# Kernel optimization log

Hardware: AMD Instinct MI355X
Metric: run time of the kernel (lower is better)

## Reference

```python
import jax, jax.numpy as jnp
import numpy as np

N, D, H, C = 100000, 128, 8, 16  # nodes, units=H*C, heads, per-head channels
E = 400000                        # edges per edge set (2 edge sets)
LN_EPS = 1e-3                     # keras LayerNormalization default epsilon


def setup_inputs() -> dict:
    key = jax.random.key(0)
    ks = jax.random.split(key, 16)
    def dense(k, i, o):
        return jax.random.normal(k, (i, o), jnp.float32) / np.float32(np.sqrt(i))
    return dict(
        x=jax.random.normal(ks[0], (N, D), jnp.float32),
        src0=jax.random.randint(ks[1], (E,), 0, N),
        dst0=jax.random.randint(ks[2], (E,), 0, N),
        src1=jax.random.randint(ks[3], (E,), 0, N),
        dst1=jax.random.randint(ks[4], (E,), 0, N),
        Wk=dense(ks[5], D, D), bk=jnp.zeros((D,), jnp.float32),
        Wm=dense(ks[6], D, D), bm=jnp.zeros((D,), jnp.float32),
        Wq=dense(ks[7], D, D), bq=jnp.zeros((D,), jnp.float32),
        Wa=dense(ks[8], D, D), ba=jnp.zeros((D,), jnp.float32),
        Watt0=jax.random.normal(ks[9], (H, C, C), jnp.float32) / np.float32(np.sqrt(C)),
        Wmsg0=jax.random.normal(ks[10], (H, C, C), jnp.float32) / np.float32(np.sqrt(C)),
        Watt1=jax.random.normal(ks[11], (H, C, C), jnp.float32) / np.float32(np.sqrt(C)),
        Wmsg1=jax.random.normal(ks[12], (H, C, C), jnp.float32) / np.float32(np.sqrt(C)),
        prior0=jnp.ones((H,), jnp.float32),
        prior1=jnp.ones((H,), jnp.float32),
        skip=jnp.ones((), jnp.float32),
        gamma=jnp.ones((D,), jnp.float32),
        beta=jnp.zeros((D,), jnp.float32),
    )


def reference(x, src0, dst0, src1, dst1, Wk, bk, Wm, bm, Wq, bq, Wa, ba,
              Watt0, Wmsg0, Watt1, Wmsg1, prior0, prior1, skip, gamma, beta):
    # Node-level projections, split per head: [N, H, C]
    k = (x @ Wk + bk).reshape(N, H, C)
    m = (x @ Wm + bm).reshape(N, H, C)
    q = (x @ Wq + bq).reshape(N, H, C)
    scale = 1.0 / jnp.sqrt(jnp.float32(C))

    def edge_terms(src, dst, Watt, Wmsg, prior):
        # per-edge-type relation projections of gathered sender keys/messages
        ke = jnp.einsum('ehk,hkl->ehl', k[src], Watt)          # [E, H, C]
        score = jnp.einsum('ehl,ehl->eh', ke, q[dst]) * prior * scale  # [E, H]
        msg = jnp.einsum('ehk,hkl->ehl', m[src], Wmsg)          # [E, H, C]
        return score, msg

    s0, m0 = edge_terms(src0, dst0, Watt0, Wmsg0, prior0)
    s1, m1 = edge_terms(src1, dst1, Watt1, Wmsg1, prior1)

    # Joint segment softmax over all incoming edges (both edge sets) per receiver
    scores = jnp.concatenate([s0, s1], axis=0)   # [2E, H]
    msgs = jnp.concatenate([m0, m1], axis=0)     # [2E, H, C]
    recv = jnp.concatenate([dst0, dst1], axis=0)

    smax = jax.ops.segment_max(scores, recv, num_segments=N)   # [N, H]
    ex = jnp.exp(scores - smax[recv])
    denom = jax.ops.segment_sum(ex, recv, num_segments=N)      # [N, H]
    d_e = denom[recv]
    attn = ex / jnp.where(d_e > 0, d_e, 1.0)                   # [2E, H]

    pooled = jax.ops.segment_sum(attn[:, :, None] * msgs, recv,
                                 num_segments=N).reshape(N, D)  # [N, D]

    # aggr(gelu(pooled)); weighted skip; layer norm
    h = jax.nn.gelu(pooled, approximate=False) @ Wa + ba
    alpha = jax.nn.sigmoid(skip)
    out = alpha * h + (1.0 - alpha) * x
    mu = jnp.mean(out, axis=-1, keepdims=True)
    var = jnp.var(out, axis=-1, keepdims=True)
    out = (out - mu) * jax.lax.rsqrt(var + LN_EPS) * gamma + beta
    return out
```

## Files before the change

### kernel.cpp

```cpp
#include <hip/hip_runtime.h>
#include <hip/hip_bf16.h>
#include <math.h>

#define N_NODES 100000
#define DIM 128
#define NH 8
#define NC 16
#define E_EDGES 400000
#define LN_EPS 1e-3f
#define SCAN_B 1024

typedef __attribute__((ext_vector_type(8))) short short8v;
typedef __attribute__((ext_vector_type(4))) float float4v;

__device__ __forceinline__ short bf16bits(float v) {
    __hip_bfloat16 b = __float2bfloat16(v);
    return *(short*)&b;
}

__global__ __launch_bounds__(128) void fuse_weights(
    const float* __restrict__ Wk, const float* __restrict__ bk,
    const float* __restrict__ Wm, const float* __restrict__ bm,
    const float* __restrict__ Wq, const float* __restrict__ bq,
    const float* __restrict__ Wa, const float* __restrict__ ba,
    const float* __restrict__ Watt0, const float* __restrict__ Wmsg0,
    const float* __restrict__ Watt1, const float* __restrict__ Wmsg1,
    const float* __restrict__ prior0, const float* __restrict__ prior1,
    __hip_bfloat16* __restrict__ Wt, float* __restrict__ bias)
{
    const int c = blockIdx.x;
    const int d = threadIdx.x;
    const int sec = c >> 7, j = c & 127, h = j >> 4, l = j & 15;
    float v, b;
    if (sec == 4)      { v = Wq[d * DIM + j]; b = bq[j]; }
    else if (sec == 5) { v = Wa[d * DIM + j]; b = ba[j]; }
    else {
        const float* W1 = (sec < 2) ? Wk : Wm;
        const float* bs = (sec < 2) ? bk : bm;
        const float* W2 = (sec == 0) ? Watt0 : (sec == 1) ? Watt1
                          : (sec == 2) ? Wmsg0 : Wmsg1;
        float scale = (sec == 0) ? prior0[h] * 0.25f
                    : (sec == 1) ? prior1[h] * 0.25f : 1.f;
        float s = 0.f, sb = 0.f;
        #pragma unroll
        for (int kk = 0; kk < NC; ++kk) {
            float w2 = W2[h * 256 + kk * 16 + l];
            s  = fmaf(W1[d * DIM + h * 16 + kk], w2, s);
            sb = fmaf(bs[h * 16 + kk], w2, sb);
        }
        v = s * scale; b = sb * scale;
    }
    Wt[(size_t)c * DIM + d] = __float2bfloat16(v);
    if (d == 0) bias[c] = b;
}

__global__ __launch_bounds__(256) void proj_mfma(
    const float* __restrict__ x,
    const __hip_bfloat16* __restrict__ Wt,
    const float* __restrict__ bias,
    __hip_bfloat16* __restrict__ kattC,
    __hip_bfloat16* __restrict__ mmsgC,
    __hip_bfloat16* __restrict__ qb)
{
    __shared__ short tile[32][DIM];
    const int wave = threadIdx.x >> 6, lane = threadIdx.x & 63;
    const int quad = lane >> 4, mcol = lane & 15;
    const int r0 = blockIdx.x * 32;

    short8v a0[4], a1[4];
    const float* xr0 = x + (size_t)(r0 + mcol) * DIM + quad * 8;
    const float* xr1 = xr0 + 16 * DIM;
    #pragma unroll
    for (int kb = 0; kb < 4; ++kb) {
        #pragma unroll
        for (int jj = 0; jj < 8; ++jj) {
            a0[kb][jj] = bf16bits(xr0[kb * 32 + jj]);
            a1[kb][jj] = bf16bits(xr1[kb * 32 + jj]);
        }
    }

    const int wrow = threadIdx.x >> 3;
    const int wcol = (threadIdx.x & 7) * 16;
    #pragma unroll
    for (int s = 0; s < 5; ++s) {
        #pragma unroll
        for (int tp = 0; tp < 2; ++tp) {
            const int ct = (wave + tp * 4) * 16;
            const int c0 = s * 128 + ct;
            const short* wp = (const short*)Wt + (size_t)(c0 + mcol) * DIM + quad * 8;
            float4v acc0 = {0.f, 0.f, 0.f, 0.f};
            float4v acc1 = {0.f, 0.f, 0.f, 0.f};
            #pragma unroll
            for (int kb = 0; kb < 4; ++kb) {
                short8v bfr = *(const short8v*)(wp + kb * 32);
                acc0 = __builtin_amdgcn_mfma_f32_16x16x32_bf16(a0[kb], bfr, acc0, 0, 0, 0);
                acc1 = __builtin_amdgcn_mfma_f32_16x16x32_bf16(a1[kb], bfr, acc1, 0, 0, 0);
            }
            const float bcol = bias[c0 + mcol];
            const int cc = ct + mcol, rq = quad * 4;
            #pragma unroll
            for (int g = 0; g < 4; ++g) {
                tile[rq + g][cc]      = bf16bits(acc0[g] + bcol);
                tile[rq + 16 + g][cc] = bf16bits(acc1[g] + bcol);
            }
        }
        __syncthreads();
        __hip_bfloat16* dst =
            (s == 0) ? kattC + (size_t)r0 * DIM :
            (s == 1) ? kattC + ((size_t)N_NODES + r0) * DIM :
            (s == 2) ? mmsgC + (size_t)r0 * DIM :
            (s == 3) ? mmsgC + ((size_t)N_NODES + r0) * DIM :
                       qb    + (size_t)r0 * DIM;
        short* dp = (short*)dst + (size_t)wrow * DIM + wcol;
        *(short8v*)dp       = *(short8v*)&tile[wrow][wcol];
        *(short8v*)(dp + 8) = *(short8v*)&tile[wrow][wcol + 8];
        __syncthreads();
    }
}

__global__ __launch_bounds__(256) void hist_kernel(
    const int* __restrict__ dst0, const int* __restrict__ dst1,
    int* __restrict__ counts)
{
    int e = blockIdx.x * 256 + threadIdx.x;
    if (e < E_EDGES) atomicAdd(&counts[dst0[e]], 1);
    int e1 = e - E_EDGES;
    if (e1 >= 0 && e1 < E_EDGES) atomicAdd(&counts[dst1[e1]], 1);
}

__global__ __launch_bounds__(SCAN_B) void scanA_kernel(
    const int* __restrict__ counts, int* __restrict__ row_ptr,
    int* __restrict__ bsum)
{
    __shared__ int buf[2][SCAN_B];
    int i = blockIdx.x * SCAN_B + threadIdx.x;
    int v = (i < N_NODES) ? counts[i] : 0;
    int cur = 0;
    buf[0][threadIdx.x] = v;
    __syncthreads();
    #pragma unroll
    for (int off = 1; off < SCAN_B; off <<= 1) {
        int t = buf[cur][threadIdx.x];
        int add = (threadIdx.x >= off) ? buf[cur][threadIdx.x - off] : 0;
        buf[cur ^ 1][threadIdx.x] = t + add;
        cur ^= 1;
        __syncthreads();
    }
    int inc = buf[cur][threadIdx.x];
    if (i < N_NODES) row_ptr[i] = inc - v;
    if (threadIdx.x == SCAN_B - 1) bsum[blockIdx.x] = inc;
}

__global__ __launch_bounds__(128) void scanB_kernel(int* __restrict__ bsum, int nblocks)
{
    __shared__ int buf[2][128];
    int t = threadIdx.x;
    int v = (t < nblocks) ? bsum[t] : 0;
    buf[0][t] = v;
    __syncthreads();
    int cur = 0;
    #pragma unroll
    for (int off = 1; off < 128; off <<= 1) {
        int a = buf[cur][t];
        if (t >= off) a += buf[cur][t - off];
        buf[cur ^ 1][t] = a;
        cur ^= 1;
        __syncthreads();
    }
    if (t < nblocks) bsum[t] = buf[cur][t] - v;
}

__global__ __launch_bounds__(SCAN_B) void scanC_kernel(
    int* __restrict__ row_ptr, int* __restrict__ cursor,
    const int* __restrict__ bsum)
{
    int i = blockIdx.x * SCAN_B + threadIdx.x;
    if (i < N_NODES) {
        int r = row_ptr[i] + bsum[blockIdx.x];
        row_ptr[i] = r;
        cursor[i] = r;
    }
}

__global__ __launch_bounds__(256) void scatter_kernel(
    const int* __restrict__ src0, const int* __restrict__ dst0,
    const int* __restrict__ src1, const int* __restrict__ dst1,
    int* __restrict__ cursor, unsigned int* __restrict__ eidx)
{
    int e = blockIdx.x * 256 + threadIdx.x;
    if (e < E_EDGES) {
        int d = dst0[e];
        int pos = atomicAdd(&cursor[d], 1);
        eidx[pos] = (unsigned int)src0[e];
    }
    int e1 = e - E_EDGES;
    if (e1 >= 0 && e1 < E_EDGES) {
        int d = dst1[e1];
        int pos = atomicAdd(&cursor[d], 1);
        eidx[pos] = (unsigned int)(src1[e1] + N_NODES);
    }
}

__global__ __launch_bounds__(256) void agg_kernel(
    const __hip_bfloat162* __restrict__ katt,
    const __hip_bfloat162* __restrict__ mmsg,
    const __hip_bfloat162* __restrict__ qb2,
    const int* __restrict__ row_ptr, const int* __restrict__ counts,
    const unsigned int* __restrict__ eidx,
    __hip_bfloat162* __restrict__ pooled2)
{
    const int wave = threadIdx.x >> 6, lane = threadIdx.x & 63;
    const int n = blockIdx.x * 4 + wave;
    if (n >= N_NODES) return;
    const int start = row_ptr[n], cnt = counts[n];
    __hip_bfloat162 qv = qb2[(size_t)n * 64 + lane];
    const float qx = __bfloat162float(qv.x), qy = __bfloat162float(qv.y);

    float accx = 0.f, accy = 0.f, den = 0.f;
    int i = 0;
    for (; i + 2 <= cnt; i += 2) {
        unsigned int r0 = eidx[start + i];
        unsigned int r1 = eidx[start + i + 1];
        __hip_bfloat162 ka0 = katt[(size_t)r0 * 64 + lane];
        __hip_bfloat162 ka1 = katt[(size_t)r1 * 64 + lane];
        __hip_bfloat162 mg0 = mmsg[(size_t)r0 * 64 + lane];
        __hip_bfloat162 mg1 = mmsg[(size_t)r1 * 64 + lane];
        float p0 = fmaf(__bfloat162float(ka0.x), qx,
                        __bfloat162float(ka0.y) * qy);
        float p1 = fmaf(__bfloat162float(ka1.x), qx,
                        __bfloat162float(ka1.y) * qy);
        p0 += __shfl_xor(p0, 1, 64); p0 += __shfl_xor(p0, 2, 64); p0 += __shfl_xor(p0, 4, 64);
        p1 += __shfl_xor(p1, 1, 64); p1 += __shfl_xor(p1, 2, 64); p1 += __shfl_xor(p1, 4, 64);
        float e0 = __expf(p0), e1 = __expf(p1);
        accx = fmaf(e0, __bfloat162float(mg0.x), accx);
        accy = fmaf(e0, __bfloat162float(mg0.y), accy);
        accx = fmaf(e1, __bfloat162float(mg1.x), accx);
        accy = fmaf(e1, __bfloat162float(mg1.y), accy);
        den += e0 + e1;
    }
    if (i < cnt) {
        unsigned int r0 = eidx[start + i];
        __hip_bfloat162 ka0 = katt[(size_t)r0 * 64 + lane];
        __hip_bfloat162 mg0 = mmsg[(size_t)r0 * 64 + lane];
        float p0 = fmaf(__bfloat162float(ka0.x), qx,
                        __bfloat162float(ka0.y) * qy);
        p0 += __shfl_xor(p0, 1, 64); p0 += __shfl_xor(p0, 2, 64); p0 += __shfl_xor(p0, 4, 64);
        float e0 = __expf(p0);
        accx = fmaf(e0, __bfloat162float(mg0.x), accx);
        accy = fmaf(e0, __bfloat162float(mg0.y), accy);
        den += e0;
    }

    float vx = 0.f, vy = 0.f;
    if (den > 0.f) { vx = accx / den; vy = accy / den; }
    vx = 0.5f * vx * (1.f + erff(vx * 0.70710678118654752f));
    vy = 0.5f * vy * (1.f + erff(vy * 0.70710678118654752f));
    __hip_bfloat162 o; o.x = __float2bfloat16(vx); o.y = __float2bfloat16(vy);
    pooled2[(size_t)n * 64 + lane] = o;
}

__global__ __launch_bounds__(256) void final_mfma(
    const __hip_bfloat16* __restrict__ pooled,
    const __hip_bfloat16* __restrict__ Wt,
    const float* __restrict__ bias,
    const float* __restrict__ x,
    const float* __restrict__ skip, const float* __restrict__ gamma,
    const float* __restrict__ beta, float* __restrict__ out)
{
    __shared__ float hs[32][DIM];
    const int wave = threadIdx.x >> 6, lane = threadIdx.x & 63;
    const int quad = lane >> 4, mcol = lane & 15;
    const int r0 = blockIdx.x * 32;

    short8v a0[4], a1[4];
    const short* pp0 = (const short*)pooled + (size_t)(r0 + mcol) * DIM + quad * 8;
    const short* pp1 = pp0 + 16 * DIM;
    #pragma unroll
    for (int kb = 0; kb < 4; ++kb) {
        a0[kb] = *(const short8v*)(pp0 + kb * 32);
        a1[kb] = *(const short8v*)(pp1 + kb * 32);
    }
    const float alpha = 1.f / (1.f + expf(-skip[0]));

    #pragma unroll
    for (int t = 0; t < 2; ++t) {
        const int c0 = wave * 32 + t * 16;
        const short* wp = (const short*)Wt + (size_t)(640 + c0 + mcol) * DIM + quad * 8;
        float4v acc0 = {0.f, 0.f, 0.f, 0.f};
        float4v acc1 = {0.f, 0.f, 0.f, 0.f};
        #pragma unroll
        for (int kb = 0; kb < 4; ++kb) {
            short8v bfr = *(const short8v*)(wp + kb * 32);
            acc0 = __builtin_amdgcn_mfma_f32_16x16x32_bf16(a0[kb], bfr, acc0, 0, 0, 0);
            acc1 = __builtin_amdgcn_mfma_f32_16x16x32_bf16(a1[kb], bfr, acc1, 0, 0, 0);
        }
        const float bcol = bias[640 + c0 + mcol];
        const int cc = c0 + mcol;
        const int rq = quad * 4;
        #pragma unroll
        for (int g = 0; g < 4; ++g) {
            int rA = rq + g, rB = rq + 16 + g;
            hs[rA][cc] = alpha * (acc0[g] + bcol)
                       + (1.f - alpha) * x[(size_t)(r0 + rA) * DIM + cc];
            hs[rB][cc] = alpha * (acc1[g] + bcol)
                       + (1.f - alpha) * x[(size_t)(r0 + rB) * DIM + cc];
        }
    }
    __syncthreads();

    float gam0 = gamma[lane], gam1 = gamma[lane + 64];
    float bet0 = beta[lane],  bet1 = beta[lane + 64];
    for (int r = wave; r < 32; r += 4) {
        int row = r0 + r;
        float v0 = hs[r][lane], v1 = hs[r][lane + 64];
        float s = v0 + v1, s2 = v0 * v0 + v1 * v1;
        #pragma unroll
        for (int off = 1; off < 64; off <<= 1) {
            s  += __shfl_xor(s,  off, 64);
            s2 += __shfl_xor(s2, off, 64);
        }
        float mu = s * (1.f / 128.f);
        float var = s2 * (1.f / 128.f) - mu * mu;
        float rstd = rsqrtf(var + LN_EPS);
        out[(size_t)row * DIM + lane]      = (v0 - mu) * rstd * gam0 + bet0;
        out[(size_t)row * DIM + lane + 64] = (v1 - mu) * rstd * gam1 + bet1;
    }
}

extern "C" void kernel_launch(void* const* d_in, const int* in_sizes, int n_in,
                              void* d_out, int out_size, void* d_ws, size_t ws_size,
                              hipStream_t stream) {
    const float* x     = (const float*)d_in[0];
    const int*   src0  = (const int*)d_in[1];
    const int*   dst0  = (const int*)d_in[2];
    const int*   src1  = (const int*)d_in[3];
    const int*   dst1  = (const int*)d_in[4];
    const float* Wk    = (const float*)d_in[5];
    const float* bk    = (const float*)d_in[6];
    const float* Wm    = (const float*)d_in[7];
    const float* bm    = (const float*)d_in[8];
    const float* Wq    = (const float*)d_in[9];
    const float* bq    = (const float*)d_in[10];
    const float* Wa    = (const float*)d_in[11];
    const float* ba    = (const float*)d_in[12];
    const float* Watt0 = (const float*)d_in[13];
    const float* Wmsg0 = (const float*)d_in[14];
    const float* Watt1 = (const float*)d_in[15];
    const float* Wmsg1 = (const float*)d_in[16];
    const float* prior0= (const float*)d_in[17];
    const float* prior1= (const float*)d_in[18];
    const float* skip  = (const float*)d_in[19];
    const float* gamma = (const float*)d_in[20];
    const float* beta  = (const float*)d_in[21];
    float* out = (float*)d_out;

    const size_t nd = (size_t)N_NODES * DIM;
    char* wsb = (char*)d_ws;
    __hip_bfloat16* Wt    = (__hip_bfloat16*)wsb;  wsb += (size_t)768 * DIM * 2;
    float* bias           = (float*)wsb;           wsb += 768 * 4;
    __hip_bfloat16* kattC = (__hip_bfloat16*)wsb;  wsb += 2 * nd * 2;
    __hip_bfloat16* mmsgC = (__hip_bfloat16*)wsb;  wsb += 2 * nd * 2;
    __hip_bfloat16* qb    = (__hip_bfloat16*)wsb;  wsb += nd * 2;
    __hip_bfloat16* pooled= (__hip_bfloat16*)wsb;  wsb += nd * 2;
    int* counts  = (int*)wsb;                      wsb += (size_t)N_NODES * 4;
    int* row_ptr = (int*)wsb;                      wsb += (size_t)N_NODES * 4;
    int* cursor  = (int*)wsb;                      wsb += (size_t)N_NODES * 4;
    int* bsum    = (int*)wsb;                      wsb += 128 * 4;
    unsigned int* eidx = (unsigned int*)wsb;

    hipMemsetAsync(counts, 0, (size_t)N_NODES * 4, stream);

    const int scan_blocks = (N_NODES + SCAN_B - 1) / SCAN_B;
    const int edge_blocks = (2 * E_EDGES + 255) / 256;

    hist_kernel<<<dim3(edge_blocks), dim3(256), 0, stream>>>(dst0, dst1, counts);
    scanA_kernel<<<dim3(scan_blocks), dim3(SCAN_B), 0, stream>>>(counts, row_ptr, bsum);
    scanB_kernel<<<dim3(1), dim3(128), 0, stream>>>(bsum, scan_blocks);
    scanC_kernel<<<dim3(scan_blocks), dim3(SCAN_B), 0, stream>>>(row_ptr, cursor, bsum);
    scatter_kernel<<<dim3(edge_blocks), dim3(256), 0, stream>>>(
        src0, dst0, src1, dst1, cursor, eidx);

    fuse_weights<<<dim3(768), dim3(128), 0, stream>>>(
        Wk, bk, Wm, bm, Wq, bq, Wa, ba,
        Watt0, Wmsg0, Watt1, Wmsg1, prior0, prior1, Wt, bias);
    proj_mfma<<<dim3(N_NODES / 32), dim3(256), 0, stream>>>(
        x, Wt, bias, kattC, mmsgC, qb);

    agg_kernel<<<dim3((N_NODES + 3) / 4), dim3(256), 0, stream>>>(
        (const __hip_bfloat162*)kattC, (const __hip_bfloat162*)mmsgC,
        (const __hip_bfloat162*)qb, row_ptr, counts, eidx,
        (__hip_bfloat162*)pooled);

    final_mfma<<<dim3(N_NODES / 32), dim3(256), 0, stream>>>(
        pooled, Wt, bias, x, skip, gamma, beta, out);
}
```

Before: 415.3 us.

## Drop scanC pass, use per-wave staging tiles, unroll aggregation loop by four

After: 420.2 us. No clear change (+1.2%).

```diff
diff --git a/kernel.cpp b/kernel.cpp
--- a/kernel.cpp
+++ b/kernel.cpp
@@ -62,31 +62,38 @@
     __hip_bfloat16* __restrict__ mmsgC,
     __hip_bfloat16* __restrict__ qb)
 {
-    __shared__ short tile[32][DIM];
+    __shared__ short tile[4][32][40];
     const int wave = threadIdx.x >> 6, lane = threadIdx.x & 63;
     const int quad = lane >> 4, mcol = lane & 15;
     const int r0 = blockIdx.x * 32;
 
     short8v a0[4], a1[4];
-    const float* xr0 = x + (size_t)(r0 + mcol) * DIM + quad * 8;
-    const float* xr1 = xr0 + 16 * DIM;
-    #pragma unroll
-    for (int kb = 0; kb < 4; ++kb) {
-        #pragma unroll
-        for (int jj = 0; jj < 8; ++jj) {
-            a0[kb][jj] = bf16bits(xr0[kb * 32 + jj]);
-            a1[kb][jj] = bf16bits(xr1[kb * 32 + jj]);
-        }
-    }
-
-    const int wrow = threadIdx.x >> 3;
-    const int wcol = (threadIdx.x & 7) * 16;
+    {
+        const float4* xp0 = (const float4*)(x + (size_t)(r0 + mcol) * DIM + quad * 8);
+        const float4* xp1 = (const float4*)(x + (size_t)(r0 + 16 + mcol) * DIM + quad * 8);
+        #pragma unroll
+        for (int kb = 0; kb < 4; ++kb) {
+            float4 u0 = xp0[kb * 8], v0 = xp0[kb * 8 + 1];
+            float4 u1 = xp1[kb * 8], v1 = xp1[kb * 8 + 1];
+            a0[kb][0] = bf16bits(u0.x); a0[kb][1] = bf16bits(u0.y);
+            a0[kb][2] = bf16bits(u0.z); a0[kb][3] = bf16bits(u0.w);
+            a0[kb][4] = bf16bits(v0.x); a0[kb][5] = bf16bits(v0.y);
+            a0[kb][6] = bf16bits(v0.z); a0[kb][7] = bf16bits(v0.w);
+            a1[kb][0] = bf16bits(u1.x); a1[kb][1] = bf16bits(u1.y);
+            a1[kb][2] = bf16bits(u1.z); a1[kb][3] = bf16bits(u1.w);
+            a1[kb][4] = bf16bits(v1.x); a1[kb][5] = bf16bits(v1.y);
+            a1[kb][6] = bf16bits(v1.z); a1[kb][7] = bf16bits(v1.w);
+        }
+    }
+
+    const int srow = lane >> 2;
+    const int scol = (lane & 3) * 8;
+
     #pragma unroll
     for (int s = 0; s < 5; ++s) {
         #pragma unroll
         for (int tp = 0; tp < 2; ++tp) {
-            const int ct = (wave + tp * 4) * 16;
-            const int c0 = s * 128 + ct;
+            const int c0 = s * 128 + wave * 32 + tp * 16;
             const short* wp = (const short*)Wt + (size_t)(c0 + mcol) * DIM + quad * 8;
             float4v acc0 = {0.f, 0.f, 0.f, 0.f};
             float4v acc1 = {0.f, 0.f, 0.f, 0.f};
@@ -97,24 +104,25 @@
                 acc1 = __builtin_amdgcn_mfma_f32_16x16x32_bf16(a1[kb], bfr, acc1, 0, 0, 0);
             }
             const float bcol = bias[c0 + mcol];
-            const int cc = ct + mcol, rq = quad * 4;
+            const int cc = tp * 16 + mcol, rq = quad * 4;
             #pragma unroll
             for (int g = 0; g < 4; ++g) {
-                tile[rq + g][cc]      = bf16bits(acc0[g] + bcol);
-                tile[rq + 16 + g][cc] = bf16bits(acc1[g] + bcol);
+                tile[wave][rq + g][cc]      = bf16bits(acc0[g] + bcol);
+                tile[wave][rq + 16 + g][cc] = bf16bits(acc1[g] + bcol);
             }
         }
-        __syncthreads();
         __hip_bfloat16* dst =
             (s == 0) ? kattC + (size_t)r0 * DIM :
             (s == 1) ? kattC + ((size_t)N_NODES + r0) * DIM :
             (s == 2) ? mmsgC + (size_t)r0 * DIM :
             (s == 3) ? mmsgC + ((size_t)N_NODES + r0) * DIM :
                        qb    + (size_t)r0 * DIM;
-        short* dp = (short*)dst + (size_t)wrow * DIM + wcol;
-        *(short8v*)dp       = *(short8v*)&tile[wrow][wcol];
-        *(short8v*)(dp + 8) = *(short8v*)&tile[wrow][wcol + 8];
-        __syncthreads();
+        #pragma unroll
+        for (int it = 0; it < 2; ++it) {
+            int row = it * 16 + srow;
+            short8v vdat = *(short8v*)&tile[wave][row][scol];
+            *(short8v*)((short*)dst + (size_t)row * DIM + wave * 32 + scol) = vdat;
+        }
     }
 }
 
@@ -170,33 +178,22 @@
     if (t < nblocks) bsum[t] = buf[cur][t] - v;
 }
 
-__global__ __launch_bounds__(SCAN_B) void scanC_kernel(
-    int* __restrict__ row_ptr, int* __restrict__ cursor,
-    const int* __restrict__ bsum)
-{
-    int i = blockIdx.x * SCAN_B + threadIdx.x;
-    if (i < N_NODES) {
-        int r = row_ptr[i] + bsum[blockIdx.x];
-        row_ptr[i] = r;
-        cursor[i] = r;
-    }
-}
-
 __global__ __launch_bounds__(256) void scatter_kernel(
     const int* __restrict__ src0, const int* __restrict__ dst0,
     const int* __restrict__ src1, const int* __restrict__ dst1,
-    int* __restrict__ cursor, unsigned int* __restrict__ eidx)
+    int* __restrict__ row_ptr, const int* __restrict__ bsum,
+    unsigned int* __restrict__ eidx)
 {
     int e = blockIdx.x * 256 + threadIdx.x;
     if (e < E_EDGES) {
         int d = dst0[e];
-        int pos = atomicAdd(&cursor[d], 1);
+        int pos = atomicAdd(&row_ptr[d], 1) + bsum[d >> 10];
         eidx[pos] = (unsigned int)src0[e];
     }
     int e1 = e - E_EDGES;
     if (e1 >= 0 && e1 < E_EDGES) {
         int d = dst1[e1];
-        int pos = atomicAdd(&cursor[d], 1);
+        int pos = atomicAdd(&row_ptr[d], 1) + bsum[d >> 10];
         eidx[pos] = (unsigned int)(src1[e1] + N_NODES);
     }
 }
@@ -206,44 +203,57 @@
     const __hip_bfloat162* __restrict__ mmsg,
     const __hip_bfloat162* __restrict__ qb2,
     const int* __restrict__ row_ptr, const int* __restrict__ counts,
+    const int* __restrict__ bsum,
     const unsigned int* __restrict__ eidx,
     __hip_bfloat162* __restrict__ pooled2)
 {
     const int wave = threadIdx.x >> 6, lane = threadIdx.x & 63;
     const int n = blockIdx.x * 4 + wave;
     if (n >= N_NODES) return;
-    const int start = row_ptr[n], cnt = counts[n];
+    const int cnt = counts[n];
+    const int start = row_ptr[n] + bsum[n >> 10] - cnt;
     __hip_bfloat162 qv = qb2[(size_t)n * 64 + lane];
     const float qx = __bfloat162float(qv.x), qy = __bfloat162float(qv.y);
 
     float accx = 0.f, accy = 0.f, den = 0.f;
     int i = 0;
-    for (; i + 2 <= cnt; i += 2) {
+    for (; i + 4 <= cnt; i += 4) {
         unsigned int r0 = eidx[start + i];
         unsigned int r1 = eidx[start + i + 1];
+        unsigned int r2 = eidx[start + i + 2];
+        unsigned int r3 = eidx[start + i + 3];
         __hip_bfloat162 ka0 = katt[(size_t)r0 * 64 + lane];
         __hip_bfloat162 ka1 = katt[(size_t)r1 * 64 + lane];
+        __hip_bfloat162 ka2 = katt[(size_t)r2 * 64 + lane];
+        __hip_bfloat162 ka3 = katt[(size_t)r3 * 64 + lane];
         __hip_bfloat162 mg0 = mmsg[(size_t)r0 * 64 + lane];
         __hip_bfloat162 mg1 = mmsg[(size_t)r1 * 64 + lane];
-        float p0 = fmaf(__bfloat162float(ka0.x), qx,
-                        __bfloat162float(ka0.y) * qy);
-        float p1 = fmaf(__bfloat162float(ka1.x), qx,
-                        __bfloat162float(ka1.y) * qy);
+        __hip_bfloat162 mg2 = mmsg[(size_t)r2 * 64 + lane];
+        __hip_bfloat162 mg3 = mmsg[(size_t)r3 * 64 + lane];
+        float p0 = fmaf(__bfloat162float(ka0.x), qx, __bfloat162float(ka0.y) * qy);
+        float p1 = fmaf(__bfloat162float(ka1.x), qx, __bfloat162float(ka1.y) * qy);
+        float p2 = fmaf(__bfloat162float(ka2.x), qx, __bfloat162float(ka2.y) * qy);
+        float p3 = fmaf(__bfloat162float(ka3.x), qx, __bfloat162float(ka3.y) * qy);
         p0 += __shfl_xor(p0, 1, 64); p0 += __shfl_xor(p0, 2, 64); p0 += __shfl_xor(p0, 4, 64);
         p1 += __shfl_xor(p1, 1, 64); p1 += __shfl_xor(p1, 2, 64); p1 += __shfl_xor(p1, 4, 64);
-        float e0 = __expf(p0), e1 = __expf(p1);
+        p2 += __shfl_xor(p2, 1, 64); p2 += __shfl_xor(p2, 2, 64); p2 += __shfl_xor(p2, 4, 64);
+        p3 += __shfl_xor(p3, 1, 64); p3 += __shfl_xor(p3, 2, 64); p3 += __shfl_xor(p3, 4, 64);
+        float e0 = __expf(p0), e1 = __expf(p1), e2 = __expf(p2), e3 = __expf(p3);
         accx = fmaf(e0, __bfloat162float(mg0.x), accx);
         accy = fmaf(e0, __bfloat162float(mg0.y), accy);
         accx = fmaf(e1, __bfloat162float(mg1.x), accx);
         accy = fmaf(e1, __bfloat162float(mg1.y), accy);
-        den += e0 + e1;
-    }
-    if (i < cnt) {
+        accx = fmaf(e2, __bfloat162float(mg2.x), accx);
+        accy = fmaf(e2, __bfloat162float(mg2.y), accy);
+        accx = fmaf(e3, __bfloat162float(mg3.x), accx);
+        accy = fmaf(e3, __bfloat162float(mg3.y), accy);
+        den += (e0 + e1) + (e2 + e3);
+    }
+    for (; i < cnt; ++i) {
         unsigned int r0 = eidx[start + i];
         __hip_bfloat162 ka0 = katt[(size_t)r0 * 64 + lane];
         __hip_bfloat162 mg0 = mmsg[(size_t)r0 * 64 + lane];
-        float p0 = fmaf(__bfloat162float(ka0.x), qx,
-                        __bfloat162float(ka0.y) * qy);
+        float p0 = fmaf(__bfloat162float(ka0.x), qx, __bfloat162float(ka0.y) * qy);
         p0 += __shfl_xor(p0, 1, 64); p0 += __shfl_xor(p0, 2, 64); p0 += __shfl_xor(p0, 4, 64);
         float e0 = __expf(p0);
         accx = fmaf(e0, __bfloat162float(mg0.x), accx);
@@ -364,7 +374,6 @@
     __hip_bfloat16* pooled= (__hip_bfloat16*)wsb;  wsb += nd * 2;
     int* counts  = (int*)wsb;                      wsb += (size_t)N_NODES * 4;
     int* row_ptr = (int*)wsb;                      wsb += (size_t)N_NODES * 4;
-    int* cursor  = (int*)wsb;                      wsb += (size_t)N_NODES * 4;
     int* bsum    = (int*)wsb;                      wsb += 128 * 4;
     unsigned int* eidx = (unsigned int*)wsb;
 
@@ -376,9 +385,8 @@
     hist_kernel<<<dim3(edge_blocks), dim3(256), 0, stream>>>(dst0, dst1, counts);
     scanA_kernel<<<dim3(scan_blocks), dim3(SCAN_B), 0, stream>>>(counts, row_ptr, bsum);
     scanB_kernel<<<dim3(1), dim3(128), 0, stream>>>(bsum, scan_blocks);
-    scanC_kernel<<<dim3(scan_blocks), dim3(SCAN_B), 0, stream>>>(row_ptr, cursor, bsum);
     scatter_kernel<<<dim3(edge_blocks), dim3(256), 0, stream>>>(
-        src0, dst0, src1, dst1, cursor, eidx);
+        src0, dst0, src1, dst1, row_ptr, bsum, eidx);
 
     fuse_weights<<<dim3(768), dim3(128), 0, stream>>>(
         Wk, bk, Wm, bm, Wq, bq, Wa, ba,
@@ -388,7 +396,7 @@
 
     agg_kernel<<<dim3((N_NODES + 3) / 4), dim3(256), 0, stream>>>(
         (const __hip_bfloat162*)kattC, (const __hip_bfloat162*)mmsgC,
-        (const __hip_bfloat162*)qb, row_ptr, counts, eidx,
+        (const __hip_bfloat162*)qb, row_ptr, counts, bsum, eidx,
         (__hip_bfloat162*)pooled);
 
     final_mfma<<<dim3(N_NODES / 32), dim3(256), 0, stream>>>(
```
